# Optimization experiments

Hardware: AMD Instinct MI355X
Metric: run time of the kernel (lower is better)

The kernel has to match this reference:

```python
import jax, jax.numpy as jnp
import numpy as np

VOCAB, D_IN, D_H, N_REL, N_CLS = 10000, 256, 256, 3, 4
N_NODES, N_EDGES, N_GRAPHS = 100000, 300000, 512


def setup_inputs() -> dict:
    key = jax.random.key(0)
    ks = jax.random.split(key, 12)
    x = jax.random.randint(ks[0], (N_NODES,), 0, VOCAB)
    edge_index = jax.random.randint(ks[1], (2, N_EDGES), 0, N_NODES)
    edge_type = jax.random.randint(ks[2], (N_EDGES,), 0, N_REL)
    batch = jnp.sort(jax.random.randint(ks[3], (N_NODES,), 0, N_GRAPHS))
    s = 0.05
    embed_table = jax.random.normal(ks[4], (VOCAB, D_IN), jnp.float32) * s
    embed_table = embed_table.at[0].set(0.0)  # padding_idx=0
    W1 = jax.random.normal(ks[5], (N_REL, D_IN, D_H), jnp.float32) * s
    root1 = jax.random.normal(ks[6], (D_IN, D_H), jnp.float32) * s
    b1 = jnp.zeros((D_H,), jnp.float32)
    W2 = jax.random.normal(ks[7], (N_REL, D_H, D_H), jnp.float32) * s
    root2 = jax.random.normal(ks[8], (D_H, D_H), jnp.float32) * s
    b2 = jnp.zeros((D_H,), jnp.float32)
    lin_W = jax.random.normal(ks[9], (D_H, N_CLS), jnp.float32) * s
    lin_b = jnp.zeros((N_CLS,), jnp.float32)
    return {"x": x, "edge_index": edge_index, "edge_type": edge_type,
            "batch": batch, "num_graphs": N_GRAPHS,
            "embed_table": embed_table, "W1": W1, "root1": root1, "b1": b1,
            "W2": W2, "root2": root2, "b2": b2, "lin_W": lin_W, "lin_b": lin_b}


def rgcn_conv(h, W, root, b, src, dst, edge_type, n_nodes):
    # PyG RGCNConv: out = h @ root + b + sum_r mean_{edges of rel r into i}(h[src] @ W_r)
    out = h @ root + b
    for r in range(W.shape[0]):
        hr = h @ W[r]                                   # [N, d_out] dense GEMM
        mask = (edge_type == r)
        msg = jnp.where(mask[:, None], hr[src], 0.0)    # [E, d_out]
        agg = jax.ops.segment_sum(msg, dst, num_segments=n_nodes)
        cnt = jax.ops.segment_sum(mask.astype(h.dtype), dst, num_segments=n_nodes)
        out = out + agg / jnp.maximum(cnt, 1.0)[:, None]
    return out


def reference(x, edge_index, edge_type, batch, num_graphs,
              embed_table, W1, root1, b1, W2, root2, b2, lin_W, lin_b):
    n_nodes = x.shape[0]
    src, dst = edge_index[0], edge_index[1]
    h = embed_table[x]                                  # [N, D_IN]
    h = jax.nn.relu(rgcn_conv(h, W1, root1, b1, src, dst, edge_type, n_nodes))
    h = jax.nn.relu(rgcn_conv(h, W2, root2, b2, src, dst, edge_type, n_nodes))
    # global mean pool by graph id
    sums = jax.ops.segment_sum(h, batch, num_segments=num_graphs)
    cnts = jax.ops.segment_sum(jnp.ones((n_nodes,), h.dtype), batch, num_segments=num_graphs)
    g = sums / jnp.maximum(cnts, 1.0)[:, None]          # [G, D_H]
    return g @ lin_W + lin_b                            # [G, N_CLS]
```

## Files before the change

kernel.cpp:

```cpp
#include <hip/hip_runtime.h>

#define D 256
#define SB 1024
typedef __attribute__((ext_vector_type(8))) short short8;
typedef __attribute__((ext_vector_type(4))) float floatx4;

__device__ __forceinline__ unsigned short f2bf(float f) {
  unsigned int u = __float_as_uint(f);
  u = (u + 0x7FFF + ((u >> 16) & 1)) >> 16;
  return (unsigned short)u;
}
__device__ __forceinline__ float bf2f(unsigned short h) {
  return __uint_as_float(((unsigned int)h) << 16);
}

__device__ __forceinline__ void glds16(const void* g, void* l) {
  __builtin_amdgcn_global_load_lds(
      (const __attribute__((address_space(1))) unsigned int*)g,
      (__attribute__((address_space(3))) unsigned int*)l, 16, 0, 0);
}

__global__ __launch_bounds__(256) void k_setup(
    int* __restrict__ cur, int RN,
    const int* __restrict__ batch, int* __restrict__ gstart, int N, int G,
    const float* __restrict__ table, unsigned short* __restrict__ tableb, int TN,
    const float* __restrict__ root1, const float* __restrict__ W1,
    const float* __restrict__ root2, const float* __restrict__ W2,
    unsigned short* __restrict__ wb, int* __restrict__ zrowi,
    int g0, int g1, int g2, int g3) {
  int b = blockIdx.x, t = threadIdx.x;
  if (b < g0) {
    int i = b * 1024 + t * 4;
#pragma unroll
    for (int j = 0; j < 4; j++) if (i + j < RN) cur[i + j] = 0;
    if (b == 0 && t < 128) zrowi[t] = 0;
  } else if (b < g1) {
    int i = (b - g0) * 256 + t;
    if (i >= N) return;
    int bb = batch[i];
    if (i == 0) { for (int g = 0; g <= bb; g++) gstart[g] = 0; }
    else { int pb = batch[i - 1]; for (int g = pb + 1; g <= bb; g++) gstart[g] = i; }
    if (i == N - 1) { for (int g = bb + 1; g <= G; g++) gstart[g] = N; }
  } else if (b < g2) {
    int i = ((b - g1) * 256 + t) * 8;
    if (i < TN) {
      float4 f0 = *(const float4*)(table + i);
      float4 f1 = *(const float4*)(table + i + 4);
      ushort4 o0, o1;
      o0.x = f2bf(f0.x); o0.y = f2bf(f0.y); o0.z = f2bf(f0.z); o0.w = f2bf(f0.w);
      o1.x = f2bf(f1.x); o1.y = f2bf(f1.y); o1.z = f2bf(f1.z); o1.w = f2bf(f1.w);
      *(ushort4*)(tableb + i) = o0;
      *(ushort4*)(tableb + i + 4) = o1;
    }
  } else {
    int layer = (b < g3) ? 0 : 1;
    int idx4 = ((b - (layer ? g3 : g2)) * 256 + t) * 4;
    int mat = idx4 >> 16, rem = idx4 & 65535;
    int n = rem >> 8, k0 = rem & 255;
    const float* root = layer ? root2 : root1;
    const float* W = layer ? W2 : W1;
    const float* s = (mat == 0) ? root : (W + (size_t)(mat - 1) * 65536);
    ushort4 o;
    o.x = f2bf(s[(k0 + 0) * 256 + n]);
    o.y = f2bf(s[(k0 + 1) * 256 + n]);
    o.z = f2bf(s[(k0 + 2) * 256 + n]);
    o.w = f2bf(s[(k0 + 3) * 256 + n]);
    *(ushort4*)(wb + (size_t)layer * 4 * 65536 + idx4) = o;
  }
}

__global__ __launch_bounds__(256) void k_count_i(const int* __restrict__ dst,
    const int* __restrict__ et, int* __restrict__ cnt, int E, int N) {
  int e = blockIdx.x * 256 + threadIdx.x;
  if (e >= E) return;
  atomicAdd(&cnt[et[e] * N + dst[e]], 1);
}

__global__ __launch_bounds__(256) void k_scan1(const int* __restrict__ in,
    int* __restrict__ bsum, int n) {
  __shared__ int s[256];
  int base = blockIdx.x * SB, t = threadIdx.x;
  int a = 0;
#pragma unroll
  for (int j = 0; j < 4; j++) { int i = base + t * 4 + j; if (i < n) a += in[i]; }
  s[t] = a; __syncthreads();
  for (int o = 128; o > 0; o >>= 1) { if (t < o) s[t] += s[t + o]; __syncthreads(); }
  if (t == 0) bsum[blockIdx.x] = s[0];
}

__global__ __launch_bounds__(256) void k_scan2(int* __restrict__ bsum, int nb,
    int* __restrict__ total_out) {
  __shared__ int s[256];
  int t = threadIdx.x;
  int v[4]; int a = 0;
#pragma unroll
  for (int j = 0; j < 4; j++) {
    int i = t * 4 + j;
    v[j] = (i < nb) ? bsum[i] : 0;
    a += v[j];
  }
  s[t] = a; __syncthreads();
  for (int o = 1; o < 256; o <<= 1) {
    int x_ = (t >= o) ? s[t - o] : 0;
    __syncthreads();
    s[t] += x_;
    __syncthreads();
  }
  int excl = (t > 0) ? s[t - 1] : 0;
#pragma unroll
  for (int j = 0; j < 4; j++) {
    int i = t * 4 + j;
    if (i < nb) { bsum[i] = excl; excl += v[j]; }
  }
  if (t == 255) *total_out = s[255];
}

__global__ __launch_bounds__(256) void k_scan3(const int* __restrict__ in,
    const int* __restrict__ bsum, int* __restrict__ off, int* __restrict__ cur,
    int n) {
  __shared__ int s[256];
  int base = blockIdx.x * SB, t = threadIdx.x;
  int v[4]; int a = 0;
#pragma unroll
  for (int j = 0; j < 4; j++) {
    int i = base + t * 4 + j;
    v[j] = (i < n) ? in[i] : 0;
    a += v[j];
  }
  s[t] = a; __syncthreads();
  for (int o = 1; o < 256; o <<= 1) {
    int x_ = (t >= o) ? s[t - o] : 0;
    __syncthreads();
    s[t] += x_;
    __syncthreads();
  }
  int excl = (t > 0 ? s[t - 1] : 0) + bsum[blockIdx.x];
#pragma unroll
  for (int j = 0; j < 4; j++) {
    int i = base + t * 4 + j;
    if (i < n) { off[i] = excl; cur[i] = excl; excl += v[j]; }
  }
}

__global__ __launch_bounds__(256) void k_place2(const int* __restrict__ src,
    const int* __restrict__ dst, const int* __restrict__ et,
    const int* __restrict__ x, int* __restrict__ cur,
    int* __restrict__ esx, int* __restrict__ ess, int E, int N) {
  int e = blockIdx.x * 256 + threadIdx.x;
  if (e >= E) return;
  int s = src[e];
  int pos = atomicAdd(&cur[et[e] * N + dst[e]], 1);
  esx[pos] = x[s];
  ess[pos] = s;
}

__global__ __launch_bounds__(256) void k_agg(const unsigned short* __restrict__ h,
    const int* __restrict__ rows, const int* __restrict__ off,
    unsigned short* __restrict__ out, int RN) {
  const int wave = threadIdx.x >> 6, lane = threadIdx.x & 63;
  const int base = (blockIdx.x * 4 + wave) * 8;
  if (base >= RN) return;

  int lo[8], hi[8];
#pragma unroll
  for (int j = 0; j < 8; j++) {
    int id = base + j;
    lo[j] = (id < RN) ? off[id] : 0;
    hi[j] = (id < RN) ? off[id + 1] : 0;
    if (hi[j] - lo[j] < 2) hi[j] = lo[j];
  }

  int r0[8];
#pragma unroll
  for (int j = 0; j < 8; j++)
    r0[j] = (hi[j] > lo[j]) ? rows[lo[j]] : 0;

  ushort4 v0[8];
#pragma unroll
  for (int j = 0; j < 8; j++)
    v0[j] = (hi[j] > lo[j])
        ? *(const ushort4*)(h + (size_t)r0[j] * D + lane * 4)
        : make_ushort4(0, 0, 0, 0);

  float a[8][4];
#pragma unroll
  for (int j = 0; j < 8; j++) {
    a[j][0] = bf2f(v0[j].x); a[j][1] = bf2f(v0[j].y);
    a[j][2] = bf2f(v0[j].z); a[j][3] = bf2f(v0[j].w);
  }

#pragma unroll
  for (int j = 0; j < 8; j++) {
    for (int p = lo[j] + 1; p < hi[j]; ++p) {
      int r = rows[p];
      ushort4 v = *(const ushort4*)(h + (size_t)r * D + lane * 4);
      a[j][0] += bf2f(v.x); a[j][1] += bf2f(v.y);
      a[j][2] += bf2f(v.z); a[j][3] += bf2f(v.w);
    }
  }

#pragma unroll
  for (int j = 0; j < 8; j++) {
    int id = base + j;
    if (id >= RN) continue;
    int c = hi[j] - lo[j];
    if (c < 2) continue;
    float inv = 1.0f / (float)c;
    ushort4 o;
    o.x = f2bf(a[j][0] * inv); o.y = f2bf(a[j][1] * inv);
    o.z = f2bf(a[j][2] * inv); o.w = f2bf(a[j][3] * inv);
    *(ushort4*)(out + (size_t)id * D + lane * 4) = o;
  }
}

__global__ __launch_bounds__(512) void k_tgemm(
    const unsigned short* __restrict__ tableb,
    const unsigned short* __restrict__ wb1,
    unsigned short* __restrict__ T, int VOCN, int nbm) {
  __shared__ unsigned short AsU[2][128 * 32];
  __shared__ unsigned short BsU[2][256 * 32];
  const int tid = threadIdx.x;
  const int w = tid >> 6, lane = tid & 63;
  const int wr = w >> 2, wc = w & 3;
  const int mat = blockIdx.x / nbm;
  const int i0 = (blockIdx.x % nbm) * 128;
  const int ml = lane & 15, q = lane >> 4;

  const int arow = w * 16 + (lane >> 2);
  const int achunk = lane & 3;
  int ra = i0 + arow;
  int rac = (ra < VOCN) ? ra : (VOCN - 1);
  const unsigned short* abase = tableb + (size_t)rac * D + achunk * 8;

  const int brow = w * 32 + (lane >> 2);
  const int bchunk = lane & 3;
  const unsigned short* bbase = wb1 + (size_t)mat * 65536
                              + (size_t)brow * D + bchunk * 8;

  floatx4 acc[4][4];
#pragma unroll
  for (int i = 0; i < 4; i++)
#pragma unroll
    for (int j = 0; j < 4; j++) acc[i][j] = (floatx4){0.f, 0.f, 0.f, 0.f};

  unsigned short* aldst[2] = {&AsU[0][w * 512], &AsU[1][w * 512]};
  unsigned short* bldst0[2] = {&BsU[0][w * 1024], &BsU[1][w * 1024]};
  unsigned short* bldst1[2] = {&BsU[0][w * 1024 + 512], &BsU[1][w * 1024 + 512]};

  for (int step = 0; step < 4; ++step) {
    __syncthreads();
#pragma unroll
    for (int h = 0; h < 2; h++) {
      const int kloc = step * 64 + h * 32;
      glds16(abase + kloc, aldst[h]);
      glds16(bbase + kloc, bldst0[h]);
      glds16(bbase + 16 * D + kloc, bldst1[h]);
    }
    __syncthreads();

#pragma unroll
    for (int h = 0; h < 2; h++) {
      short8 aF[4], bF[4];
#pragma unroll
      for (int mi = 0; mi < 4; mi++)
        aF[mi] = *(const short8*)&AsU[h][(wr * 64 + mi * 16 + ml) * 32 + q * 8];
#pragma unroll
      for (int ni = 0; ni < 4; ni++)
        bF[ni] = *(const short8*)&BsU[h][(wc * 64 + ni * 16 + ml) * 32 + q * 8];
#pragma unroll
      for (int mi = 0; mi < 4; mi++)
#pragma unroll
        for (int ni = 0; ni < 4; ni++)
          acc[mi][ni] = __builtin_amdgcn_mfma_f32_16x16x32_bf16(
              aF[mi], bF[ni], acc[mi][ni], 0, 0, 0);
    }
  }

#pragma unroll
  for (int mi = 0; mi < 4; mi++) {
#pragma unroll
    for (int ni = 0; ni < 4; ni++) {
      int col = wc * 64 + ni * 16 + ml;
#pragma unroll
      for (int j = 0; j < 4; j++) {
        int row = i0 + wr * 64 + mi * 16 + q * 4 + j;
        if (row < VOCN)
          T[((size_t)mat * VOCN + row) * D + col] = f2bf(acc[mi][ni][j]);
      }
    }
  }
}

__global__ __launch_bounds__(256) void k_combine(
    const int* __restrict__ x, const int* __restrict__ esx,
    const int* __restrict__ off, const unsigned short* __restrict__ T,
    const float* __restrict__ bias, unsigned short* __restrict__ outP,
    int N, int VOCN) {
  const int wave = threadIdx.x >> 6, lane = threadIdx.x & 63;
  const int base = (blockIdx.x * 4 + wave) * 2;
  if (base >= N) return;
  float4 bv = *(const float4*)(bias + lane * 4);

  int id[2];
  id[0] = base;
  id[1] = (base + 1 < N) ? (base + 1) : base;

  ushort4 rv[2];
  int lo[2][3], hi[2][3];
#pragma unroll
  for (int u = 0; u < 2; u++) {
    rv[u] = *(const ushort4*)(T + (size_t)x[id[u]] * D + lane * 4);
#pragma unroll
    for (int r = 0; r < 3; r++) {
      lo[u][r] = off[r * N + id[u]];
      hi[u][r] = off[r * N + id[u] + 1];
    }
  }
  ushort4 f[2][3];
#pragma unroll
  for (int u = 0; u < 2; u++)
#pragma unroll
    for (int r = 0; r < 3; r++)
      f[u][r] = (hi[u][r] > lo[u][r])
          ? *(const ushort4*)(T + ((size_t)(r + 1) * VOCN + esx[lo[u][r]]) * D
                              + lane * 4)
          : make_ushort4(0, 0, 0, 0);

#pragma unroll
  for (int u = 0; u < 2; u++) {
    float a0 = bf2f(rv[u].x) + bv.x, a1 = bf2f(rv[u].y) + bv.y;
    float a2 = bf2f(rv[u].z) + bv.z, a3 = bf2f(rv[u].w) + bv.w;
#pragma unroll
    for (int r = 0; r < 3; r++) {
      int c = hi[u][r] - lo[u][r];
      if (c <= 0) continue;
      float s0 = bf2f(f[u][r].x), s1 = bf2f(f[u][r].y);
      float s2 = bf2f(f[u][r].z), s3 = bf2f(f[u][r].w);
      for (int p = lo[u][r] + 1; p < hi[u][r]; ++p) {
        ushort4 w = *(const ushort4*)(T + ((size_t)(r + 1) * VOCN + esx[p]) * D
                                      + lane * 4);
        s0 += bf2f(w.x); s1 += bf2f(w.y); s2 += bf2f(w.z); s3 += bf2f(w.w);
      }
      float inv = 1.0f / (float)c;
      a0 += s0 * inv; a1 += s1 * inv; a2 += s2 * inv; a3 += s3 * inv;
    }
    ushort4 o;
    o.x = f2bf(fmaxf(a0, 0.f)); o.y = f2bf(fmaxf(a1, 0.f));
    o.z = f2bf(fmaxf(a2, 0.f)); o.w = f2bf(fmaxf(a3, 0.f));
    *(ushort4*)(outP + (size_t)id[u] * D + lane * 4) = o;
  }
}

__global__ __launch_bounds__(512) void k_lgemm(
    const unsigned short* __restrict__ Aroot, const int* __restrict__ gidx,
    const unsigned short* agg, const int* __restrict__ rows_,
    const int* __restrict__ off_, const unsigned short* __restrict__ zrow,
    const unsigned short* __restrict__ wb,
    const float* __restrict__ bias, unsigned short* Cout, int M, int N) {
  __shared__ unsigned short AsU[2][128 * 32];
  __shared__ unsigned short BsU[2][256 * 32];
  const int tid = threadIdx.x;
  const int w = tid >> 6, lane = tid & 63;
  const int wr = w >> 2, wc = w & 3;
  const int i0 = blockIdx.x * 128;
  const int ml = lane & 15, q = lane >> 4;

  const int arow = w * 16 + (lane >> 2);
  const int achunk = lane & 3;
  int ra = i0 + arow;
  int rac = (ra < M) ? ra : (M - 1);
  const int rowA0 = gidx ? gidx[rac] : rac;
  const unsigned short* abase[4];
  abase[0] = Aroot + (size_t)rowA0 * D + achunk * 8;
#pragma unroll
  for (int r = 0; r < 3; r++) {
    int id = r * N + rac;
    int lo = off_[id];
    int cnt = off_[id + 1] - lo;
    const unsigned short* b;
    if (cnt == 0) b = zrow;
    else if (cnt == 1) b = Aroot + (size_t)rows_[lo] * D;
    else b = agg + (size_t)id * D;
    abase[r + 1] = b + achunk * 8;
  }

  const int brow = w * 32 + (lane >> 2);
  const int bchunk = lane & 3;
  const size_t bofs = (size_t)brow * D + bchunk * 8;

  floatx4 acc[4][4];
#pragma unroll
  for (int i = 0; i < 4; i++)
#pragma unroll
    for (int j = 0; j < 4; j++) acc[i][j] = (floatx4){0.f, 0.f, 0.f, 0.f};

  unsigned short* aldst[2] = {&AsU[0][w * 512], &AsU[1][w * 512]};
  unsigned short* bldst0[2] = {&BsU[0][w * 1024], &BsU[1][w * 1024]};
  unsigned short* bldst1[2] = {&BsU[0][w * 1024 + 512], &BsU[1][w * 1024 + 512]};

  for (int step = 0; step < 16; ++step) {
    __syncthreads();
#pragma unroll
    for (int h = 0; h < 2; h++) {
      const int kabs = step * 64 + h * 32;
      const int seg = kabs >> 8, kloc = kabs & 255;
      glds16(abase[seg] + kloc, aldst[h]);
      const unsigned short* bb = wb + (size_t)seg * 65536 + bofs + kloc;
      glds16(bb, bldst0[h]);
      glds16(bb + 16 * D, bldst1[h]);
    }
    __syncthreads();

#pragma unroll
    for (int h = 0; h < 2; h++) {
      short8 aF[4], bF[4];
#pragma unroll
      for (int mi = 0; mi < 4; mi++)
        aF[mi] = *(const short8*)&AsU[h][(wr * 64 + mi * 16 + ml) * 32 + q * 8];
#pragma unroll
      for (int ni = 0; ni < 4; ni++)
        bF[ni] = *(const short8*)&BsU[h][(wc * 64 + ni * 16 + ml) * 32 + q * 8];
#pragma unroll
      for (int mi = 0; mi < 4; mi++)
#pragma unroll
        for (int ni = 0; ni < 4; ni++)
          acc[mi][ni] = __builtin_amdgcn_mfma_f32_16x16x32_bf16(
              aF[mi], bF[ni], acc[mi][ni], 0, 0, 0);
    }
  }

  __syncthreads();

  float bv[4];
#pragma unroll
  for (int ni = 0; ni < 4; ni++) bv[ni] = bias[wc * 64 + ni * 16 + ml];
#pragma unroll
  for (int mi = 0; mi < 4; mi++) {
#pragma unroll
    for (int ni = 0; ni < 4; ni++) {
      int col = wc * 64 + ni * 16 + ml;
#pragma unroll
      for (int j = 0; j < 4; j++) {
        int row = i0 + wr * 64 + mi * 16 + q * 4 + j;
        if (row < M) {
          float v = fmaxf(acc[mi][ni][j] + bv[ni], 0.f);
          Cout[(size_t)row * D + col] = f2bf(v);
        }
      }
    }
  }
}

__global__ __launch_bounds__(256) void k_poolfinal(
    const unsigned short* __restrict__ h, const int* __restrict__ gstart,
    const float* __restrict__ linW, const float* __restrict__ linb,
    float* __restrict__ out, int G) {
  __shared__ float red[4][D];
  __shared__ float sred[4][4];
  int g = blockIdx.x;
  int lo = gstart[g], hi = gstart[g + 1];
  int tid = threadIdx.x, wave = tid >> 6, lane = tid & 63;
  float a0 = 0.f, a1 = 0.f, a2 = 0.f, a3 = 0.f;
  for (int i = lo + wave; i < hi; i += 4) {
    ushort4 v = *(const ushort4*)(h + (size_t)i * D + lane * 4);
    a0 += bf2f(v.x); a1 += bf2f(v.y); a2 += bf2f(v.z); a3 += bf2f(v.w);
  }
  red[wave][lane * 4 + 0] = a0;
  red[wave][lane * 4 + 1] = a1;
  red[wave][lane * 4 + 2] = a2;
  red[wave][lane * 4 + 3] = a3;
  __syncthreads();
  float s = red[0][tid] + red[1][tid] + red[2][tid] + red[3][tid];
  float inv = (hi > lo) ? 1.0f / (float)(hi - lo) : 0.0f;
  float m = s * inv;
  float4 wrow = *(const float4*)(linW + tid * 4);
  float p0 = m * wrow.x, p1 = m * wrow.y, p2 = m * wrow.z, p3 = m * wrow.w;
  for (int o = 32; o > 0; o >>= 1) {
    p0 += __shfl_down(p0, o, 64);
    p1 += __shfl_down(p1, o, 64);
    p2 += __shfl_down(p2, o, 64);
    p3 += __shfl_down(p3, o, 64);
  }
  if (lane == 0) {
    sred[wave][0] = p0; sred[wave][1] = p1;
    sred[wave][2] = p2; sred[wave][3] = p3;
  }
  __syncthreads();
  if (tid < 4)
    out[g * 4 + tid] = sred[0][tid] + sred[1][tid] + sred[2][tid] +
                       sred[3][tid] + linb[tid];
}

extern "C" void kernel_launch(void* const* d_in, const int* in_sizes, int n_in,
                              void* d_out, int out_size, void* d_ws, size_t ws_size,
                              hipStream_t stream) {
  const int*   x     = (const int*)d_in[0];
  const int*   ei    = (const int*)d_in[1];
  const int*   et    = (const int*)d_in[2];
  const int*   batch = (const int*)d_in[3];
  const float* table = (const float*)d_in[5];
  const float* W1    = (const float*)d_in[6];
  const float* root1 = (const float*)d_in[7];
  const float* b1    = (const float*)d_in[8];
  const float* W2    = (const float*)d_in[9];
  const float* root2 = (const float*)d_in[10];
  const float* b2    = (const float*)d_in[11];
  const float* linW  = (const float*)d_in[12];
  const float* linb  = (const float*)d_in[13];
  float* out = (float*)d_out;

  const int N = in_sizes[0];
  const int E = in_sizes[2];
  const int G = out_size / 4;
  const int VOC = in_sizes[5] / D;
  const int* src = ei;
  const int* dst = ei + E;
  const int RN = 3 * N;

  char* wsb = (char*)d_ws;
  size_t pg = (size_t)N * D * 2;
  unsigned short* P0 = (unsigned short*)wsb;
  unsigned short* P1 = (unsigned short*)(wsb + pg);
  unsigned short* P3 = (unsigned short*)(wsb + 3 * pg);
  unsigned short* wb = (unsigned short*)(wsb + 4 * pg);
  unsigned short* zrow = wb + 2 * 4 * 65536;
  int*   off    = (int*)(zrow + 256);
  int*   esx    = off + (RN + 1);
  int*   ess    = esx + E;
  int*   gstart = ess + E;
  unsigned short* tableb = P3;
  unsigned short* Tbuf = P1;
  int* cur  = (int*)P0;
  int* bsum = cur + RN;

  const int nb = (RN + SB - 1) / SB;

  int nbZero = (RN + 1023) / 1024;
  int nbBounds = (N + 255) / 256;
  int nbCvt = (VOC * D / 8 + 255) / 256;
  int g0 = nbZero, g1 = g0 + nbBounds, g2 = g1 + nbCvt, g3 = g2 + 256;
  k_setup<<<g3 + 256, 256, 0, stream>>>(cur, RN, batch, gstart, N, G,
      table, tableb, VOC * D, root1, W1, root2, W2, wb, (int*)zrow,
      g0, g1, g2, g3);

  const int nbm = (VOC + 127) / 128;
  k_tgemm<<<nbm * 4, 512, 0, stream>>>(tableb, wb, Tbuf, VOC, nbm);

  k_count_i<<<(E + 255) / 256, 256, 0, stream>>>(dst, et, cur, E, N);
  k_scan1<<<nb, 256, 0, stream>>>(cur, bsum, RN);
  k_scan2<<<1, 256, 0, stream>>>(bsum, nb, off + RN);
  k_scan3<<<nb, 256, 0, stream>>>(cur, bsum, off, cur, RN);
  k_place2<<<(E + 255) / 256, 256, 0, stream>>>(src, dst, et, x, cur, esx, ess, E, N);

  k_combine<<<(N + 7) / 8, 256, 0, stream>>>(x, esx, off, Tbuf, b1, P0, N, VOC);

  const int gagg = (RN + 31) / 32;
  const int ggemm = (N + 127) / 128;

  k_agg<<<gagg, 256, 0, stream>>>(P0, ess, off, P1, RN);
  k_lgemm<<<ggemm, 512, 0, stream>>>(P0, nullptr, P1, ess, off, zrow,
                                     wb + 4 * 65536, b2, P1, N, N);

  k_poolfinal<<<G, 256, 0, stream>>>(P1, gstart, linW, linb, out, G);
}
```

Baseline: 323.2 us.

## Fuse global mean pooling into layer-2 GEMM epilogue via atomics

The second RGCN GEMM no longer writes the bf16 hidden tensor. Its epilogue reduces ReLU outputs per graph id, in LDS when a tile spans at most four graphs and with direct atomics otherwise, and atomically adds the sums into a float per-graph buffer. A small kernel then divides by node counts and applies the final linear layer. This removes the N×256 write and reread of the layer-2 output, at the cost of a zeroing kernel, float atomics whose order is nondeterministic, and reuse of the esx workspace region for the graph sums.

New measurement: 348.0 us. +7.7%, slower.

```diff
diff --git a/kernel.cpp b/kernel.cpp
--- a/kernel.cpp
+++ b/kernel.cpp
@@ -213,6 +213,11 @@
   }
 }
 
+__global__ __launch_bounds__(256) void k_zerog(float* __restrict__ gsum, int n4) {
+  int i = blockIdx.x * 256 + threadIdx.x;
+  if (i < n4) ((float4*)gsum)[i] = make_float4(0.f, 0.f, 0.f, 0.f);
+}
+
 __global__ __launch_bounds__(512) void k_tgemm(
     const unsigned short* __restrict__ tableb,
     const unsigned short* __restrict__ wb1,
@@ -356,7 +361,8 @@
     const unsigned short* agg, const int* __restrict__ rows_,
     const int* __restrict__ off_, const unsigned short* __restrict__ zrow,
     const unsigned short* __restrict__ wb,
-    const float* __restrict__ bias, unsigned short* Cout, int M, int N) {
+    const float* __restrict__ bias, unsigned short* __restrict__ Cout,
+    const int* __restrict__ batchv, float* __restrict__ gsum, int M, int N) {
   __shared__ unsigned short AsU[2][128 * 32];
   __shared__ unsigned short BsU[2][256 * 32];
   const int tid = threadIdx.x;
@@ -434,47 +440,97 @@
   float bv[4];
 #pragma unroll
   for (int ni = 0; ni < 4; ni++) bv[ni] = bias[wc * 64 + ni * 16 + ml];
-#pragma unroll
-  for (int mi = 0; mi < 4; mi++) {
-#pragma unroll
-    for (int ni = 0; ni < 4; ni++) {
-      int col = wc * 64 + ni * 16 + ml;
+
+  if (gsum) {
+    int lastrow = (i0 + 127 < M) ? (i0 + 127) : (M - 1);
+    int gfirst = batchv[(i0 < M) ? i0 : (M - 1)];
+    int glast = batchv[lastrow];
+    int nspan = glast - gfirst + 1;
+    int gb[4][4];
+#pragma unroll
+    for (int mi = 0; mi < 4; mi++)
 #pragma unroll
       for (int j = 0; j < 4; j++) {
         int row = i0 + wr * 64 + mi * 16 + q * 4 + j;
-        if (row < M) {
-          float v = fmaxf(acc[mi][ni][j] + bv[ni], 0.f);
-          Cout[(size_t)row * D + col] = f2bf(v);
+        gb[mi][j] = (row < M) ? batchv[row] : -1;
+      }
+    if (nspan <= 4) {
+      float* lred = (float*)&BsU[0][0];
+      const int slot = wr * 4 + q;
+      for (int gl = 0; gl < nspan; gl++) {
+        int g = gfirst + gl;
+#pragma unroll
+        for (int ni = 0; ni < 4; ni++) {
+          float s = 0.f;
+#pragma unroll
+          for (int mi = 0; mi < 4; mi++)
+#pragma unroll
+            for (int j = 0; j < 4; j++)
+              if (gb[mi][j] == g)
+                s += fmaxf(acc[mi][ni][j] + bv[ni], 0.f);
+          int col = wc * 64 + ni * 16 + ml;
+          lred[(slot * 4 + gl) * 256 + col] = s;
         }
       }
-    }
-  }
-}
-
-__global__ __launch_bounds__(256) void k_poolfinal(
-    const unsigned short* __restrict__ h, const int* __restrict__ gstart,
+      __syncthreads();
+      for (int idx = tid; idx < nspan * 256; idx += 512) {
+        int gl = idx >> 8, col = idx & 255;
+        float s = 0.f;
+#pragma unroll
+        for (int sl = 0; sl < 8; sl++)
+          s += lred[(sl * 4 + gl) * 256 + col];
+        atomicAdd(&gsum[(size_t)(gfirst + gl) * D + col], s);
+      }
+    } else {
+#pragma unroll
+      for (int mi = 0; mi < 4; mi++)
+#pragma unroll
+        for (int j = 0; j < 4; j++) {
+          if (gb[mi][j] < 0) continue;
+#pragma unroll
+          for (int ni = 0; ni < 4; ni++) {
+            int col = wc * 64 + ni * 16 + ml;
+            atomicAdd(&gsum[(size_t)gb[mi][j] * D + col],
+                      fmaxf(acc[mi][ni][j] + bv[ni], 0.f));
+          }
+        }
+    }
+  } else {
+#pragma unroll
+    for (int mi = 0; mi < 4; mi++) {
+#pragma unroll
+      for (int ni = 0; ni < 4; ni++) {
+        int col = wc * 64 + ni * 16 + ml;
+#pragma unroll
+        for (int j = 0; j < 4; j++) {
+          int row = i0 + wr * 64 + mi * 16 + q * 4 + j;
+          if (row < M) {
+            float v = fmaxf(acc[mi][ni][j] + bv[ni], 0.f);
+            Cout[(size_t)row * D + col] = f2bf(v);
+          }
+        }
+      }
+    }
+  }
+}
+
+__global__ __launch_bounds__(64) void k_final(
+    const float* __restrict__ gsum, const int* __restrict__ gstart,
     const float* __restrict__ linW, const float* __restrict__ linb,
     float* __restrict__ out, int G) {
-  __shared__ float red[4][D];
-  __shared__ float sred[4][4];
-  int g = blockIdx.x;
-  int lo = gstart[g], hi = gstart[g + 1];
-  int tid = threadIdx.x, wave = tid >> 6, lane = tid & 63;
-  float a0 = 0.f, a1 = 0.f, a2 = 0.f, a3 = 0.f;
-  for (int i = lo + wave; i < hi; i += 4) {
-    ushort4 v = *(const ushort4*)(h + (size_t)i * D + lane * 4);
-    a0 += bf2f(v.x); a1 += bf2f(v.y); a2 += bf2f(v.z); a3 += bf2f(v.w);
-  }
-  red[wave][lane * 4 + 0] = a0;
-  red[wave][lane * 4 + 1] = a1;
-  red[wave][lane * 4 + 2] = a2;
-  red[wave][lane * 4 + 3] = a3;
-  __syncthreads();
-  float s = red[0][tid] + red[1][tid] + red[2][tid] + red[3][tid];
-  float inv = (hi > lo) ? 1.0f / (float)(hi - lo) : 0.0f;
-  float m = s * inv;
-  float4 wrow = *(const float4*)(linW + tid * 4);
-  float p0 = m * wrow.x, p1 = m * wrow.y, p2 = m * wrow.z, p3 = m * wrow.w;
+  int g = blockIdx.x, lane = threadIdx.x;
+  int cnt = gstart[g + 1] - gstart[g];
+  float inv = (cnt > 0) ? 1.0f / (float)cnt : 0.0f;
+  float4 s = *(const float4*)(gsum + (size_t)g * D + lane * 4);
+  float m0 = s.x * inv, m1 = s.y * inv, m2 = s.z * inv, m3 = s.w * inv;
+  float4 w0 = *(const float4*)(linW + (lane * 4 + 0) * 4);
+  float4 w1 = *(const float4*)(linW + (lane * 4 + 1) * 4);
+  float4 w2 = *(const float4*)(linW + (lane * 4 + 2) * 4);
+  float4 w3 = *(const float4*)(linW + (lane * 4 + 3) * 4);
+  float p0 = m0 * w0.x + m1 * w1.x + m2 * w2.x + m3 * w3.x;
+  float p1 = m0 * w0.y + m1 * w1.y + m2 * w2.y + m3 * w3.y;
+  float p2 = m0 * w0.z + m1 * w1.z + m2 * w2.z + m3 * w3.z;
+  float p3 = m0 * w0.w + m1 * w1.w + m2 * w2.w + m3 * w3.w;
   for (int o = 32; o > 0; o >>= 1) {
     p0 += __shfl_down(p0, o, 64);
     p1 += __shfl_down(p1, o, 64);
@@ -482,13 +538,11 @@
     p3 += __shfl_down(p3, o, 64);
   }
   if (lane == 0) {
-    sred[wave][0] = p0; sred[wave][1] = p1;
-    sred[wave][2] = p2; sred[wave][3] = p3;
-  }
-  __syncthreads();
-  if (tid < 4)
-    out[g * 4 + tid] = sred[0][tid] + sred[1][tid] + sred[2][tid] +
-                       sred[3][tid] + linb[tid];
+    out[g * 4 + 0] = p0 + linb[0];
+    out[g * 4 + 1] = p1 + linb[1];
+    out[g * 4 + 2] = p2 + linb[2];
+    out[g * 4 + 3] = p3 + linb[3];
+  }
 }
 
 extern "C" void kernel_launch(void* const* d_in, const int* in_sizes, int n_in,
@@ -532,6 +586,7 @@
   unsigned short* Tbuf = P1;
   int* cur  = (int*)P0;
   int* bsum = cur + RN;
+  float* gsum = (float*)((((size_t)esx) + 15) & ~(size_t)15);
 
   const int nb = (RN + SB - 1) / SB;
 
@@ -554,12 +609,15 @@
 
   k_combine<<<(N + 7) / 8, 256, 0, stream>>>(x, esx, off, Tbuf, b1, P0, N, VOC);
 
+  k_zerog<<<(G * D / 4 + 255) / 256, 256, 0, stream>>>(gsum, G * D / 4);
+
   const int gagg = (RN + 31) / 32;
   const int ggemm = (N + 127) / 128;
 
   k_agg<<<gagg, 256, 0, stream>>>(P0, ess, off, P1, RN);
   k_lgemm<<<ggemm, 512, 0, stream>>>(P0, nullptr, P1, ess, off, zrow,
-                                     wb + 4 * 65536, b2, P1, N, N);
-
-  k_poolfinal<<<G, 256, 0, stream>>>(P1, gstart, linW, linb, out, G);
-}
+                                     wb + 4 * 65536, b2, nullptr, batch, gsum,
+                                     N, N);
+
+  k_final<<<G, 64, 0, stream>>>(gsum, gstart, linW, linb, out, G);
+}
```
